# Kernel optimization log

Hardware: AMD Instinct MI355X
Metric: run time of the kernel (lower is better)

Reference implementation:

```python
import jax, jax.numpy as jnp
import numpy as np

N = 50000        # nodes
E = 800000       # edges (before self loops)
F_IN = 64        # num_features
DIM = 64         # num_hidden
C = 10           # num_classes
G = 256          # graphs in batch
NEG_SLOPE = 0.2


def setup_inputs() -> dict:
    key = jax.random.key(0)
    ks = jax.random.split(key, 20)
    def w(k, shape, fan_in):
        return jax.random.normal(k, shape, dtype=jnp.float32) / np.sqrt(fan_in)
    x = jax.random.normal(ks[0], (N, F_IN), dtype=jnp.float32)
    edge_index = jax.random.randint(ks[1], (2, E), 0, N, dtype=jnp.int64)
    batch = jnp.sort(jax.random.randint(ks[2], (N,), 0, G, dtype=jnp.int64))
    return {
        "x": x, "edge_index": edge_index, "batch": batch,
        "w1": w(ks[3], (F_IN, DIM), F_IN), "as1": w(ks[4], (DIM,), DIM), "ad1": w(ks[5], (DIM,), DIM), "b1": jnp.zeros((DIM,), jnp.float32),
        "w2": w(ks[6], (DIM, DIM), DIM),  "as2": w(ks[7], (DIM,), DIM), "ad2": w(ks[8], (DIM,), DIM), "b2": jnp.zeros((DIM,), jnp.float32),
        "w3": w(ks[9], (DIM, DIM), DIM),  "as3": w(ks[10], (DIM,), DIM), "ad3": w(ks[11], (DIM,), DIM), "b3": jnp.zeros((DIM,), jnp.float32),
        "fc1_w": w(ks[12], (DIM, DIM), DIM), "fc1_b": jnp.zeros((DIM,), jnp.float32),
        "fc2_w": w(ks[13], (DIM, C), DIM),   "fc2_b": jnp.zeros((C,), jnp.float32),
    }


def _gat_conv(x, src, dst, w, a_src, a_dst, b, n_nodes):
    # PyG GATConv, heads=1: h = x W; e_ij = LeakyReLU(a_src.h_j + a_dst.h_i);
    # alpha = segment-softmax over edges grouped by target i; out_i = sum_j alpha_ij h_j + b
    h = x @ w                                   # [N, DIM]
    alpha_s = h @ a_src                         # [N]
    alpha_d = h @ a_dst                         # [N]
    e = jax.nn.leaky_relu(alpha_s[src] + alpha_d[dst], NEG_SLOPE)  # [E']
    e_max = jax.ops.segment_max(e, dst, num_segments=n_nodes)
    e_exp = jnp.exp(e - e_max[dst])
    denom = jax.ops.segment_sum(e_exp, dst, num_segments=n_nodes)
    alpha = e_exp / (denom[dst] + 1e-16)        # [E']
    out = jax.ops.segment_sum(alpha[:, None] * h[src], dst, num_segments=n_nodes)
    return out + b


def _l2_normalize(x):
    nrm = jnp.linalg.norm(x, axis=1, keepdims=True)
    return x / jnp.maximum(nrm, 1e-12)


def reference(x, edge_index, batch, w1, as1, ad1, b1, w2, as2, ad2, b2,
              w3, as3, ad3, b3, fc1_w, fc1_b, fc2_w, fc2_b):
    n = x.shape[0]
    loops = jnp.arange(n, dtype=edge_index.dtype)
    src = jnp.concatenate([edge_index[0], loops])   # add_self_loops=True (PyG default)
    dst = jnp.concatenate([edge_index[1], loops])
    h = _gat_conv(x, src, dst, w1, as1, ad1, b1, n)
    h = jax.nn.relu(_l2_normalize(h))
    h = _gat_conv(h, src, dst, w2, as2, ad2, b2, n)
    h = jax.nn.relu(_l2_normalize(h))
    h = _gat_conv(h, src, dst, w3, as3, ad3, b3, n)
    h = jax.nn.relu(_l2_normalize(h))
    g = jax.ops.segment_sum(h, batch, num_segments=G)   # global_add_pool -> [G, DIM]
    g = jax.nn.relu(g @ fc1_w + fc1_b)
    logits = g @ fc2_w + fc2_b
    return jax.nn.log_softmax(logits, axis=-1)
```

## Files before the change

kernel.cpp:

```cpp
#include <hip/hip_runtime.h>
#include <hip/hip_bf16.h>
#include <math.h>

#define DIM 64
#define GNUM 256
#define CNUM 10

__device__ __forceinline__ unsigned bfpack(float a, float b) {
    unsigned ua = __builtin_bit_cast(unsigned, a);
    unsigned ub = __builtin_bit_cast(unsigned, b);
    ua += 0x7fffu + ((ua >> 16) & 1u);
    ub += 0x7fffu + ((ub >> 16) & 1u);
    return (ua >> 16) | (ub & 0xffff0000u);
}
__device__ __forceinline__ float bflo(unsigned u) { return __builtin_bit_cast(float, u << 16); }
__device__ __forceinline__ float bfhi(unsigned u) { return __builtin_bit_cast(float, u & 0xffff0000u); }
__device__ __forceinline__ float bfs(unsigned short u) { return __builtin_bit_cast(float, (unsigned)u << 16); }

__global__ void deg_rank_kernel(const int* __restrict__ ei, int E, int N,
                                int* __restrict__ deg, int* __restrict__ rank) {
    int i = blockIdx.x * blockDim.x + threadIdx.x;
    int EP = E + N;
    if (i >= EP) return;
    int d = (i < E) ? ei[E + i] : (i - E);
    rank[i] = atomicAdd(&deg[d], 1);
}

__global__ __launch_bounds__(256) void scan_misc(const int* __restrict__ deg, int* __restrict__ part, int n, int nb,
                                                 const int* __restrict__ batch, int N,
                                                 int* __restrict__ gstart) {
    int bid = blockIdx.x;
    if (bid < nb) {
        __shared__ int ws[4];
        int i = bid * 256 + threadIdx.x;
        int v = (i < n) ? deg[i] : 0;
        #pragma unroll
        for (int d = 32; d >= 1; d >>= 1) v += __shfl_xor(v, d);
        if ((threadIdx.x & 63) == 0) ws[threadIdx.x >> 6] = v;
        __syncthreads();
        if (threadIdx.x == 0) part[bid] = ws[0] + ws[1] + ws[2] + ws[3];
    } else {
        for (int g = threadIdx.x; g <= GNUM; g += 256) {
            int lo = 0, hi = N;
            while (lo < hi) { int mid = (lo + hi) >> 1; if (batch[mid] < g) lo = mid + 1; else hi = mid; }
            gstart[g] = lo;
        }
    }
}

__global__ __launch_bounds__(256) void scan_down(const int* __restrict__ deg, const int* __restrict__ part,
                                                 int* __restrict__ offs, int n) {
    __shared__ int ws[4];
    __shared__ int base_s;
    int tid = threadIdx.x, lane = tid & 63, wid = tid >> 6;
    int pv = (tid < (int)blockIdx.x) ? part[tid] : 0;
    #pragma unroll
    for (int d = 32; d >= 1; d >>= 1) pv += __shfl_xor(pv, d);
    if (lane == 0) ws[wid] = pv;
    __syncthreads();
    if (tid == 0) base_s = ws[0] + ws[1] + ws[2] + ws[3];
    __syncthreads();
    int i = blockIdx.x * 256 + tid;
    int v = (i < n) ? deg[i] : 0;
    int x = v;
    #pragma unroll
    for (int d = 1; d < 64; d <<= 1) { int t = __shfl_up(x, d); if (lane >= d) x += t; }
    if (lane == 63) ws[wid] = x;
    __syncthreads();
    int add = base_s;
    for (int w = 0; w < wid; ++w) add += ws[w];
    if (i < n) offs[i] = add + x - v;
    if (i == n - 1) offs[n] = add + x;
}

#define XSTR 68
__device__ __forceinline__ void mm_core_512(const float* __restrict__ xT, const float* __restrict__ Ws,
                                            const float* __restrict__ a_s, const float* __restrict__ a_d,
                                            unsigned* __restrict__ hbn, float* __restrict__ asn,
                                            float* __restrict__ adn, int base, int N) {
    int tid = threadIdx.x;
    int tx = tid & 15, ty = tid >> 4;
    int c0 = tx << 2, r0 = ty << 1;
    float acc[2][4] = {{0.f}};
    #pragma unroll 8
    for (int k = 0; k < DIM; ++k) {
        float2 xv = *(const float2*)(xT + k * XSTR + r0);
        float4 wv = *(const float4*)(Ws + k * DIM + c0);
        acc[0][0] += xv.x * wv.x; acc[0][1] += xv.x * wv.y; acc[0][2] += xv.x * wv.z; acc[0][3] += xv.x * wv.w;
        acc[1][0] += xv.y * wv.x; acc[1][1] += xv.y * wv.y; acc[1][2] += xv.y * wv.z; acc[1][3] += xv.y * wv.w;
    }
    float4 av = *(const float4*)(a_s + c0);
    float4 dv = *(const float4*)(a_d + c0);
    #pragma unroll
    for (int ri = 0; ri < 2; ++ri) {
        int grow = base + r0 + ri;
        float s1 = acc[ri][0] * av.x + acc[ri][1] * av.y + acc[ri][2] * av.z + acc[ri][3] * av.w;
        float s2 = acc[ri][0] * dv.x + acc[ri][1] * dv.y + acc[ri][2] * dv.z + acc[ri][3] * dv.w;
        #pragma unroll
        for (int d = 1; d <= 8; d <<= 1) { s1 += __shfl_xor(s1, d); s2 += __shfl_xor(s2, d); }
        if (grow < N) {
            uint2 o;
            o.x = bfpack(acc[ri][0], acc[ri][1]);
            o.y = bfpack(acc[ri][2], acc[ri][3]);
            *(uint2*)(hbn + ((size_t)grow << 5) + (tx << 1)) = o;
            if (tx == 0) { asn[grow] = s1; adn[grow] = s2; }
        }
    }
}

__global__ __launch_bounds__(512) void mm_fill(const float* __restrict__ in, const float* __restrict__ W,
                                               const float* __restrict__ a_s, const float* __restrict__ a_d,
                                               unsigned* __restrict__ hb, float* __restrict__ as_,
                                               float* __restrict__ ad_, int N, int nbt,
                                               const int* __restrict__ ei, const int* __restrict__ rank, int E,
                                               const int* __restrict__ offs, int2* __restrict__ csr_sd) {
    int bid = blockIdx.x;
    if (bid < nbt) {
        __shared__ float Ws[DIM * DIM];
        __shared__ float xT[XSTR * DIM];
        int tid = threadIdx.x;
        int base = bid * 64;

        const float4* W4 = (const float4*)W;
        float4* Ws4 = (float4*)Ws;
        Ws4[tid] = W4[tid];
        Ws4[tid + 512] = W4[tid + 512];

        {
            int row = tid >> 3;
            int kb = (tid & 7) << 3;
            int grow = base + row;
            int crow = grow < N ? grow : N - 1;
            const float4* xr = (const float4*)(in + ((size_t)crow << 6) + kb);
            float4 v0 = xr[0], v1 = xr[1];
            xT[(kb + 0) * XSTR + row] = v0.x;  xT[(kb + 1) * XSTR + row] = v0.y;
            xT[(kb + 2) * XSTR + row] = v0.z;  xT[(kb + 3) * XSTR + row] = v0.w;
            xT[(kb + 4) * XSTR + row] = v1.x;  xT[(kb + 5) * XSTR + row] = v1.y;
            xT[(kb + 6) * XSTR + row] = v1.z;  xT[(kb + 7) * XSTR + row] = v1.w;
        }
        __syncthreads();
        mm_core_512(xT, Ws, a_s, a_d, hb, as_, ad_, base, N);
    } else {
        int i = (bid - nbt) * 512 + threadIdx.x;
        int EP = E + N;
        if (i >= EP) return;
        int s, d;
        if (i < E) { s = ei[i]; d = ei[E + i]; } else { s = i - E; d = i - E; }
        csr_sd[offs[d] + rank[i]] = make_int2(s, d);
    }
}

#define FUS_NPB 64
#define FUS_CAP 2560
__global__ __launch_bounds__(512) void agg_mm(const unsigned* __restrict__ hbp,
                                              const int2* __restrict__ csr_sd,
                                              const float* __restrict__ asp,
                                              const float* __restrict__ adp,
                                              const int* __restrict__ offs,
                                              const float* __restrict__ bias,
                                              const float* __restrict__ W,
                                              const float* __restrict__ a_s,
                                              const float* __restrict__ a_d,
                                              unsigned* __restrict__ hbn,
                                              float* __restrict__ asn,
                                              float* __restrict__ adn, int N) {
    __shared__ int soffs[FUS_NPB + 1];
    __shared__ float adl[FUS_NPB];
    __shared__ int2 lsw[FUS_CAP + 4];
    __shared__ float xT[XSTR * DIM];
    float* Ws = (float*)lsw;

    int tid = threadIdx.x;
    int base = blockIdx.x * FUS_NPB;
    if (tid <= FUS_NPB) {
        int n = base + tid;
        soffs[tid] = offs[n < N ? n : N];
    }
    if (tid < FUS_NPB) {
        int n = base + tid;
        adl[tid] = (n < N) ? adp[n] : 0.f;
    }
    __syncthreads();
    int estart = soffs[0];
    int nE = soffs[FUS_NPB] - estart;
    bool inLds = (nE <= FUS_CAP);
    if (inLds) {
        for (int i = tid; i < nE; i += 512) {
            int2 sd = csr_sd[estart + i];
            float e = asp[sd.x] + adl[sd.y - base];
            e = (e > 0.f) ? e : 0.2f * e;
            lsw[i] = make_int2(sd.x, __builtin_bit_cast(int, expf(e)));
        }
        if (tid < 4) lsw[nE + tid] = make_int2(0, 0);
    }
    __syncthreads();

    int li = tid >> 3, fg = tid & 7;
    int node = base + li;
    int ls = soffs[li] - estart;
    int deg = soffs[li + 1] - soffs[li];

    float a0 = 0.f, a1 = 0.f, a2 = 0.f, a3 = 0.f;
    float a4 = 0.f, a5 = 0.f, a6 = 0.f, a7 = 0.f, sw = 0.f;
    if (inLds) {
        for (int eb = 0; eb < deg; eb += 4) {
            int t = ls + eb;
            int2 eA = lsw[t], eB = lsw[t + 1], eC = lsw[t + 2], eD = lsw[t + 3];
            float wA = __builtin_bit_cast(float, eA.y);
            float wB = (eb + 1 < deg) ? __builtin_bit_cast(float, eB.y) : 0.f;
            float wC = (eb + 2 < deg) ? __builtin_bit_cast(float, eC.y) : 0.f;
            float wD = (eb + 3 < deg) ? __builtin_bit_cast(float, eD.y) : 0.f;
            const uint4 hA = *(const uint4*)(hbp + ((size_t)eA.x << 5) + (fg << 2));
            const uint4 hB = *(const uint4*)(hbp + ((size_t)eB.x << 5) + (fg << 2));
            const uint4 hC = *(const uint4*)(hbp + ((size_t)eC.x << 5) + (fg << 2));
            const uint4 hD = *(const uint4*)(hbp + ((size_t)eD.x << 5) + (fg << 2));
            sw += wA + wB + wC + wD;
            a0 += wA * bflo(hA.x) + wB * bflo(hB.x) + wC * bflo(hC.x) + wD * bflo(hD.x);
            a1 += wA * bfhi(hA.x) + wB * bfhi(hB.x) + wC * bfhi(hC.x) + wD * bfhi(hD.x);
            a2 += wA * bflo(hA.y) + wB * bflo(hB.y) + wC * bflo(hC.y) + wD * bflo(hD.y);
            a3 += wA * bfhi(hA.y) + wB * bfhi(hB.y) + wC * bfhi(hC.y) + wD * bfhi(hD.y);
            a4 += wA * bflo(hA.z) + wB * bflo(hB.z) + wC * bflo(hC.z) + wD * bflo(hD.z);
            a5 += wA * bfhi(hA.z) + wB * bfhi(hB.z) + wC * bfhi(hC.z) + wD * bfhi(hD.z);
            a6 += wA * bflo(hA.w) + wB * bflo(hB.w) + wC * bflo(hC.w) + wD * bflo(hD.w);
            a7 += wA * bfhi(hA.w) + wB * bfhi(hB.w) + wC * bfhi(hC.w) + wD * bfhi(hD.w);
        }
    } else {
        float adi = adl[li];
        for (int eb = 0; eb < deg; eb += 4) {
            int t = estart + ls + eb;
            float wv[4]; int sv[4];
            #pragma unroll
            for (int k = 0; k < 4; ++k) {
                int2 sd = (eb + k < deg) ? csr_sd[t + k] : make_int2(0, 0);
                int s = sd.x; s = s < 0 ? 0 : (s >= N ? N - 1 : s);
                float e = asp[s] + adi;
                e = (e > 0.f) ? e : 0.2f * e;
                wv[k] = (eb + k < deg) ? expf(e) : 0.f;
                sv[k] = s;
            }
            #pragma unroll
            for (int k = 0; k < 4; ++k) {
                const uint4 hv = *(const uint4*)(hbp + ((size_t)sv[k] << 5) + (fg << 2));
                sw += wv[k];
                a0 += wv[k] * bflo(hv.x); a1 += wv[k] * bfhi(hv.x);
                a2 += wv[k] * bflo(hv.y); a3 += wv[k] * bfhi(hv.y);
                a4 += wv[k] * bflo(hv.z); a5 += wv[k] * bfhi(hv.z);
                a6 += wv[k] * bflo(hv.w); a7 += wv[k] * bfhi(hv.w);
            }
        }
    }

    float inv = 1.f / (sw + 1e-16f);
    const float4 b0 = *(const float4*)(bias + (fg << 3));
    const float4 b1 = *(const float4*)(bias + (fg << 3) + 4);
    float o0 = a0 * inv + b0.x, o1 = a1 * inv + b0.y, o2 = a2 * inv + b0.z, o3 = a3 * inv + b0.w;
    float o4 = a4 * inv + b1.x, o5 = a5 * inv + b1.y, o6 = a6 * inv + b1.z, o7 = a7 * inv + b1.w;
    float n2 = o0 * o0 + o1 * o1 + o2 * o2 + o3 * o3 + o4 * o4 + o5 * o5 + o6 * o6 + o7 * o7;
    #pragma unroll
    for (int d = 1; d <= 4; d <<= 1) n2 += __shfl_xor(n2, d);
    float innrm = 1.f / fmaxf(sqrtf(n2), 1e-12f);
    if (node >= N) innrm = 0.f;
    int kb = fg << 3;
    xT[(kb + 0) * XSTR + li] = fmaxf(o0 * innrm, 0.f);
    xT[(kb + 1) * XSTR + li] = fmaxf(o1 * innrm, 0.f);
    xT[(kb + 2) * XSTR + li] = fmaxf(o2 * innrm, 0.f);
    xT[(kb + 3) * XSTR + li] = fmaxf(o3 * innrm, 0.f);
    xT[(kb + 4) * XSTR + li] = fmaxf(o4 * innrm, 0.f);
    xT[(kb + 5) * XSTR + li] = fmaxf(o5 * innrm, 0.f);
    xT[(kb + 6) * XSTR + li] = fmaxf(o6 * innrm, 0.f);
    xT[(kb + 7) * XSTR + li] = fmaxf(o7 * innrm, 0.f);
    __syncthreads();

    const float4* W4 = (const float4*)W;
    float4* Ws4 = (float4*)Ws;
    Ws4[tid] = W4[tid];
    Ws4[tid + 512] = W4[tid + 512];
    __syncthreads();
    mm_core_512(xT, Ws, a_s, a_d, hbn, asn, adn, base, N);
}

#define AGG_NPB 64
#define AGG_CAP 2560
__global__ __launch_bounds__(512) void gat_agg(const unsigned* __restrict__ hb,
                                               const int2* __restrict__ csr_sd,
                                               const float* __restrict__ as_,
                                               const float* __restrict__ ad_,
                                               const int* __restrict__ offs,
                                               const float* __restrict__ bias,
                                               unsigned* __restrict__ outb, int N) {
    __shared__ int soffs[AGG_NPB + 1];
    __shared__ float adl[AGG_NPB];
    __shared__ int2 lsw[AGG_CAP + 4];
    int tid = threadIdx.x;
    int base = blockIdx.x * AGG_NPB;
    if (tid <= AGG_NPB) {
        int n = base + tid;
        soffs[tid] = offs[n < N ? n : N];
    }
    if (tid < AGG_NPB) {
        int n = base + tid;
        adl[tid] = (n < N) ? ad_[n] : 0.f;
    }
    __syncthreads();
    int estart = soffs[0];
    int nE = soffs[AGG_NPB] - estart;
    bool inLds = (nE <= AGG_CAP);
    if (inLds) {
        for (int i = tid; i < nE; i += 512) {
            int2 sd = csr_sd[estart + i];
            float e = as_[sd.x] + adl[sd.y - base];
            e = (e > 0.f) ? e : 0.2f * e;
            lsw[i] = make_int2(sd.x, __builtin_bit_cast(int, expf(e)));
        }
        if (tid < 4) lsw[nE + tid] = make_int2(0, 0);
    }
    __syncthreads();

    int li = tid >> 3, fg = tid & 7;
    int node = base + li;
    int ls = soffs[li] - estart;
    int deg = soffs[li + 1] - soffs[li];

    float a0 = 0.f, a1 = 0.f, a2 = 0.f, a3 = 0.f;
    float a4 = 0.f, a5 = 0.f, a6 = 0.f, a7 = 0.f, sw = 0.f;
    if (inLds) {
        for (int eb = 0; eb < deg; eb += 4) {
            int t = ls + eb;
            int2 eA = lsw[t], eB = lsw[t + 1], eC = lsw[t + 2], eD = lsw[t + 3];
            float wA = __builtin_bit_cast(float, eA.y);
            float wB = (eb + 1 < deg) ? __builtin_bit_cast(float, eB.y) : 0.f;
            float wC = (eb + 2 < deg) ? __builtin_bit_cast(float, eC.y) : 0.f;
            float wD = (eb + 3 < deg) ? __builtin_bit_cast(float, eD.y) : 0.f;
            const uint4 hA = *(const uint4*)(hb + ((size_t)eA.x << 5) + (fg << 2));
            const uint4 hB = *(const uint4*)(hb + ((size_t)eB.x << 5) + (fg << 2));
            const uint4 hC = *(const uint4*)(hb + ((size_t)eC.x << 5) + (fg << 2));
            const uint4 hD = *(const uint4*)(hb + ((size_t)eD.x << 5) + (fg << 2));
            sw += wA + wB + wC + wD;
            a0 += wA * bflo(hA.x) + wB * bflo(hB.x) + wC * bflo(hC.x) + wD * bflo(hD.x);
            a1 += wA * bfhi(hA.x) + wB * bfhi(hB.x) + wC * bfhi(hC.x) + wD * bfhi(hD.x);
            a2 += wA * bflo(hA.y) + wB * bflo(hB.y) + wC * bflo(hC.y) + wD * bflo(hD.y);
            a3 += wA * bfhi(hA.y) + wB * bfhi(hB.y) + wC * bfhi(hC.y) + wD * bfhi(hD.y);
            a4 += wA * bflo(hA.z) + wB * bflo(hB.z) + wC * bflo(hC.z) + wD * bflo(hD.z);
            a5 += wA * bfhi(hA.z) + wB * bfhi(hB.z) + wC * bfhi(hC.z) + wD * bfhi(hD.z);
            a6 += wA * bflo(hA.w) + wB * bflo(hB.w) + wC * bflo(hC.w) + wD * bflo(hD.w);
            a7 += wA * bfhi(hA.w) + wB * bfhi(hB.w) + wC * bfhi(hC.w) + wD * bfhi(hD.w);
        }
    } else {
        float adi = (node < N) ? ad_[node] : 0.f;
        for (int eb = 0; eb < deg; eb += 4) {
            int t = estart + ls + eb;
            float wv[4]; int sv[4];
            #pragma unroll
            for (int k = 0; k < 4; ++k) {
                int2 sd = (eb + k < deg) ? csr_sd[t + k] : make_int2(0, 0);
                int s = sd.x; s = s < 0 ? 0 : (s >= N ? N - 1 : s);
                float e = as_[s] + adi;
                e = (e > 0.f) ? e : 0.2f * e;
                wv[k] = (eb + k < deg) ? expf(e) : 0.f;
                sv[k] = s;
            }
            #pragma unroll
            for (int k = 0; k < 4; ++k) {
                const uint4 hv = *(const uint4*)(hb + ((size_t)sv[k] << 5) + (fg << 2));
                sw += wv[k];
                a0 += wv[k] * bflo(hv.x); a1 += wv[k] * bfhi(hv.x);
                a2 += wv[k] * bflo(hv.y); a3 += wv[k] * bfhi(hv.y);
                a4 += wv[k] * bflo(hv.z); a5 += wv[k] * bfhi(hv.z);
                a6 += wv[k] * bflo(hv.w); a7 += wv[k] * bfhi(hv.w);
            }
        }
    }

    float inv = 1.f / (sw + 1e-16f);
    const float4 b0 = *(const float4*)(bias + (fg << 3));
    const float4 b1 = *(const float4*)(bias + (fg << 3) + 4);
    float o0 = a0 * inv + b0.x, o1 = a1 * inv + b0.y, o2 = a2 * inv + b0.z, o3 = a3 * inv + b0.w;
    float o4 = a4 * inv + b1.x, o5 = a5 * inv + b1.y, o6 = a6 * inv + b1.z, o7 = a7 * inv + b1.w;
    float n2 = o0 * o0 + o1 * o1 + o2 * o2 + o3 * o3 + o4 * o4 + o5 * o5 + o6 * o6 + o7 * o7;
    #pragma unroll
    for (int d = 1; d <= 4; d <<= 1) n2 += __shfl_xor(n2, d);
    float innrm = 1.f / fmaxf(sqrtf(n2), 1e-12f);
    if (node < N) {
        uint4 o;
        o.x = bfpack(fmaxf(o0 * innrm, 0.f), fmaxf(o1 * innrm, 0.f));
        o.y = bfpack(fmaxf(o2 * innrm, 0.f), fmaxf(o3 * innrm, 0.f));
        o.z = bfpack(fmaxf(o4 * innrm, 0.f), fmaxf(o5 * innrm, 0.f));
        o.w = bfpack(fmaxf(o6 * innrm, 0.f), fmaxf(o7 * innrm, 0.f));
        *(uint4*)(outb + ((size_t)node << 5) + (fg << 2)) = o;
    }
}

__global__ __launch_bounds__(256) void pool_mlp(const unsigned short* __restrict__ hb, const int* __restrict__ gstart,
                                                const float* __restrict__ fc1w, const float* __restrict__ fc1b,
                                                const float* __restrict__ fc2w, const float* __restrict__ fc2b,
                                                float* __restrict__ out) {
    __shared__ float W1[DIM * DIM];
    __shared__ float red[4 * DIM];
    __shared__ float tbuf[DIM];
    __shared__ float obuf[CNUM];
    int tid = threadIdx.x, lane = tid & 63, wv = tid >> 6;
    int gid = blockIdx.x;

    const float4* W4 = (const float4*)fc1w;
    float4* W1s = (float4*)W1;
    #pragma unroll
    for (int i = 0; i < 4; ++i) W1s[tid + 256 * i] = W4[tid + 256 * i];

    int s = gstart[gid], e = gstart[gid + 1];
    float acc = 0.f;
    for (int i = s + wv; i < e; i += 4) acc += bfs(hb[((size_t)i << 6) + lane]);
    red[wv * DIM + lane] = acc;
    __syncthreads();

    if (wv == 0) {
        float g = red[lane] + red[DIM + lane] + red[2 * DIM + lane] + red[3 * DIM + lane];
        float t = fc1b[lane];
        #pragma unroll
        for (int k = 0; k < DIM; ++k) t += __shfl(g, k) * W1[k * DIM + lane];
        t = fmaxf(t, 0.f);
        tbuf[lane] = t;
        float o = 0.f;
        if (lane < CNUM) {
            o = fc2b[lane];
            #pragma unroll
            for (int k = 0; k < DIM; ++k) o += tbuf[k] * fc2w[k * CNUM + lane];
            obuf[lane] = o;
        }
        if (lane < CNUM) {
            float mx = obuf[0];
            #pragma unroll
            for (int k = 1; k < CNUM; ++k) mx = fmaxf(mx, obuf[k]);
            float ssum = 0.f;
            #pragma unroll
            for (int k = 0; k < CNUM; ++k) ssum += expf(obuf[k] - mx);
            out[gid * CNUM + lane] = o - mx - logf(ssum);
        }
    }
}

static inline size_t align256(size_t x) { return (x + 255) & ~size_t(255); }

extern "C" void kernel_launch(void* const* d_in, const int* in_sizes, int n_in,
                              void* d_out, int out_size, void* d_ws, size_t ws_size,
                              hipStream_t stream) {
    const float* x     = (const float*)d_in[0];
    const int*   ei    = (const int*)d_in[1];
    const int*   batch = (const int*)d_in[2];
    const float* w1  = (const float*)d_in[3];
    const float* as1 = (const float*)d_in[4];
    const float* ad1 = (const float*)d_in[5];
    const float* b1  = (const float*)d_in[6];
    const float* w2  = (const float*)d_in[7];
    const float* as2 = (const float*)d_in[8];
    const float* ad2 = (const float*)d_in[9];
    const float* b2  = (const float*)d_in[10];
    const float* w3  = (const float*)d_in[11];
    const float* as3 = (const float*)d_in[12];
    const float* ad3 = (const float*)d_in[13];
    const float* b3  = (const float*)d_in[14];
    const float* fc1w = (const float*)d_in[15];
    const float* fc1b = (const float*)d_in[16];
    const float* fc2w = (const float*)d_in[17];
    const float* fc2b = (const float*)d_in[18];
    float* out = (float*)d_out;

    int N  = in_sizes[0] / DIM;
    int E  = in_sizes[1] / 2;
    int EP = E + N;
    int nb = (N + 255) / 256;

    char* p = (char*)d_ws;
    unsigned* hbA = (unsigned*)p; p += align256(sizeof(unsigned) * (size_t)N * (DIM / 2));
    unsigned* hbB = (unsigned*)p; p += align256(sizeof(unsigned) * (size_t)N * (DIM / 2));
    unsigned* oAb = (unsigned*)p; p += align256(sizeof(unsigned) * (size_t)N * (DIM / 2));
    float* asA  = (float*)p; p += align256(sizeof(float) * (size_t)N);
    float* adA  = (float*)p; p += align256(sizeof(float) * (size_t)N);
    float* asB  = (float*)p; p += align256(sizeof(float) * (size_t)N);
    float* adB  = (float*)p; p += align256(sizeof(float) * (size_t)N);
    int*   deg  = (int*)p;   p += align256(sizeof(int) * (size_t)N);
    int*   offs = (int*)p;   p += align256(sizeof(int) * (size_t)(N + 1));
    int*   rank = (int*)p;   p += align256(sizeof(int) * (size_t)EP);
    int2*  csr_sd = (int2*)p; p += align256(sizeof(int2) * (size_t)EP);
    int*   part = (int*)p;   p += align256(sizeof(int) * (size_t)nb);
    int*   gst  = (int*)p;   p += align256(sizeof(int) * (size_t)(GNUM + 1));

    int nfb  = (N + FUS_NPB - 1) / FUS_NPB;
    int nblk = (N + AGG_NPB - 1) / AGG_NPB;
    int nbt = (N + 63) / 64;
    int epBlocks = (EP + 511) / 512;

    hipMemsetAsync(deg, 0, sizeof(int) * (size_t)N, stream);
    deg_rank_kernel<<<(EP + 255) / 256, 256, 0, stream>>>(ei, E, N, deg, rank);
    scan_misc<<<nb + 1, 256, 0, stream>>>(deg, part, N, nb, batch, N, gst);
    scan_down<<<nb, 256, 0, stream>>>(deg, part, offs, N);

    mm_fill<<<nbt + epBlocks, 512, 0, stream>>>(x, w1, as1, ad1, hbA, asA, adA, N, nbt,
                                                ei, rank, E, offs, csr_sd);
    agg_mm<<<nfb, 512, 0, stream>>>(hbA, csr_sd, asA, adA, offs, b1, w2, as2, ad2,
                                    hbB, asB, adB, N);
    agg_mm<<<nfb, 512, 0, stream>>>(hbB, csr_sd, asB, adB, offs, b2, w3, as3, ad3,
                                    hbA, asA, adA, N);
    gat_agg<<<nblk, 512, 0, stream>>>(hbA, csr_sd, asA, adA, offs, b3, oAb, N);

    pool_mlp<<<GNUM, 256, 0, stream>>>((const unsigned short*)oAb, gst, fc1w, fc1b, fc2w, fc2b, out);
}
```

Before: 253.5 us.

## Fuse last GAT aggregation with global pooling and MLP head via atomics

```diff
diff --git a/kernel.cpp b/kernel.cpp
--- a/kernel.cpp
+++ b/kernel.cpp
@@ -15,7 +15,6 @@
 }
 __device__ __forceinline__ float bflo(unsigned u) { return __builtin_bit_cast(float, u << 16); }
 __device__ __forceinline__ float bfhi(unsigned u) { return __builtin_bit_cast(float, u & 0xffff0000u); }
-__device__ __forceinline__ float bfs(unsigned short u) { return __builtin_bit_cast(float, (unsigned)u << 16); }
 
 __global__ void deg_rank_kernel(const int* __restrict__ ei, int E, int N,
                                 int* __restrict__ deg, int* __restrict__ rank) {
@@ -279,20 +278,63 @@
     mm_core_512(xT, Ws, a_s, a_d, hbn, asn, adn, base, N);
 }
 
+__device__ __forceinline__ void mlp_wave(int g, float gv, int lane,
+                                         const float* __restrict__ fc1w, const float* __restrict__ fc1b,
+                                         const float* __restrict__ fc2w, const float* __restrict__ fc2b,
+                                         float* __restrict__ out) {
+    float t = fc1b[lane];
+    #pragma unroll 8
+    for (int k = 0; k < DIM; ++k) t += __shfl(gv, k) * fc1w[k * DIM + lane];
+    t = fmaxf(t, 0.f);
+    float o = (lane < CNUM) ? fc2b[lane] : 0.f;
+    #pragma unroll 8
+    for (int k = 0; k < DIM; ++k) {
+        float tk = __shfl(t, k);
+        if (lane < CNUM) o += tk * fc2w[k * CNUM + lane];
+    }
+    float mx = -1e30f;
+    #pragma unroll
+    for (int c = 0; c < CNUM; ++c) mx = fmaxf(mx, __shfl(o, c));
+    float ss = 0.f;
+    #pragma unroll
+    for (int c = 0; c < CNUM; ++c) ss += expf(__shfl(o, c) - mx);
+    if (lane < CNUM) out[g * CNUM + lane] = o - mx - logf(ss);
+}
+
 #define AGG_NPB 64
 #define AGG_CAP 2560
-__global__ __launch_bounds__(512) void gat_agg(const unsigned* __restrict__ hb,
-                                               const int2* __restrict__ csr_sd,
-                                               const float* __restrict__ as_,
-                                               const float* __restrict__ ad_,
-                                               const int* __restrict__ offs,
-                                               const float* __restrict__ bias,
-                                               unsigned* __restrict__ outb, int N) {
+__global__ __launch_bounds__(512) void agg_pool(const unsigned* __restrict__ hb,
+                                                const int2* __restrict__ csr_sd,
+                                                const float* __restrict__ as_,
+                                                const float* __restrict__ ad_,
+                                                const int* __restrict__ offs,
+                                                const float* __restrict__ bias,
+                                                const int* __restrict__ batch,
+                                                const int* __restrict__ gstart,
+                                                float* __restrict__ gbuf,
+                                                int* __restrict__ gcnt,
+                                                const float* __restrict__ fc1w, const float* __restrict__ fc1b,
+                                                const float* __restrict__ fc2w, const float* __restrict__ fc2b,
+                                                float* __restrict__ out, int N, int nblk) {
+    if ((int)blockIdx.x == nblk) {
+        if (threadIdx.x < 64) {
+            int lane = threadIdx.x;
+            for (int g = 0; g < GNUM; ++g)
+                if (gstart[g + 1] == gstart[g])
+                    mlp_wave(g, 0.f, lane, fc1w, fc1b, fc2w, fc2b, out);
+        }
+        return;
+    }
     __shared__ int soffs[AGG_NPB + 1];
     __shared__ float adl[AGG_NPB];
     __shared__ int2 lsw[AGG_CAP + 4];
+    __shared__ float nodeout[64 * 66];
+    __shared__ int bgr[64];
+    __shared__ int fing[64];
+    __shared__ int nfin;
     int tid = threadIdx.x;
     int base = blockIdx.x * AGG_NPB;
+    if (tid == 0) nfin = 0;
     if (tid <= AGG_NPB) {
         int n = base + tid;
         soffs[tid] = offs[n < N ? n : N];
@@ -300,6 +342,7 @@
     if (tid < AGG_NPB) {
         int n = base + tid;
         adl[tid] = (n < N) ? ad_[n] : 0.f;
+        bgr[tid] = (n < N) ? batch[n] : -1;
     }
     __syncthreads();
     int estart = soffs[0];
@@ -346,7 +389,7 @@
             a7 += wA * bfhi(hA.w) + wB * bfhi(hB.w) + wC * bfhi(hC.w) + wD * bfhi(hD.w);
         }
     } else {
-        float adi = (node < N) ? ad_[node] : 0.f;
+        float adi = adl[li];
         for (int eb = 0; eb < deg; eb += 4) {
             int t = estart + ls + eb;
             float wv[4]; int sv[4];
@@ -380,60 +423,50 @@
     #pragma unroll
     for (int d = 1; d <= 4; d <<= 1) n2 += __shfl_xor(n2, d);
     float innrm = 1.f / fmaxf(sqrtf(n2), 1e-12f);
-    if (node < N) {
-        uint4 o;
-        o.x = bfpack(fmaxf(o0 * innrm, 0.f), fmaxf(o1 * innrm, 0.f));
-        o.y = bfpack(fmaxf(o2 * innrm, 0.f), fmaxf(o3 * innrm, 0.f));
-        o.z = bfpack(fmaxf(o4 * innrm, 0.f), fmaxf(o5 * innrm, 0.f));
-        o.w = bfpack(fmaxf(o6 * innrm, 0.f), fmaxf(o7 * innrm, 0.f));
-        *(uint4*)(outb + ((size_t)node << 5) + (fg << 2)) = o;
-    }
-}
-
-__global__ __launch_bounds__(256) void pool_mlp(const unsigned short* __restrict__ hb, const int* __restrict__ gstart,
-                                                const float* __restrict__ fc1w, const float* __restrict__ fc1b,
-                                                const float* __restrict__ fc2w, const float* __restrict__ fc2b,
-                                                float* __restrict__ out) {
-    __shared__ float W1[DIM * DIM];
-    __shared__ float red[4 * DIM];
-    __shared__ float tbuf[DIM];
-    __shared__ float obuf[CNUM];
-    int tid = threadIdx.x, lane = tid & 63, wv = tid >> 6;
-    int gid = blockIdx.x;
-
-    const float4* W4 = (const float4*)fc1w;
-    float4* W1s = (float4*)W1;
-    #pragma unroll
-    for (int i = 0; i < 4; ++i) W1s[tid + 256 * i] = W4[tid + 256 * i];
-
-    int s = gstart[gid], e = gstart[gid + 1];
-    float acc = 0.f;
-    for (int i = s + wv; i < e; i += 4) acc += bfs(hb[((size_t)i << 6) + lane]);
-    red[wv * DIM + lane] = acc;
-    __syncthreads();
-
-    if (wv == 0) {
-        float g = red[lane] + red[DIM + lane] + red[2 * DIM + lane] + red[3 * DIM + lane];
-        float t = fc1b[lane];
-        #pragma unroll
-        for (int k = 0; k < DIM; ++k) t += __shfl(g, k) * W1[k * DIM + lane];
-        t = fmaxf(t, 0.f);
-        tbuf[lane] = t;
-        float o = 0.f;
-        if (lane < CNUM) {
-            o = fc2b[lane];
-            #pragma unroll
-            for (int k = 0; k < DIM; ++k) o += tbuf[k] * fc2w[k * CNUM + lane];
-            obuf[lane] = o;
-        }
-        if (lane < CNUM) {
-            float mx = obuf[0];
-            #pragma unroll
-            for (int k = 1; k < CNUM; ++k) mx = fmaxf(mx, obuf[k]);
-            float ssum = 0.f;
-            #pragma unroll
-            for (int k = 0; k < CNUM; ++k) ssum += expf(obuf[k] - mx);
-            out[gid * CNUM + lane] = o - mx - logf(ssum);
+    if (node >= N) innrm = 0.f;
+    int co = fg << 3;
+    nodeout[li * 66 + co + 0] = fmaxf(o0 * innrm, 0.f);
+    nodeout[li * 66 + co + 1] = fmaxf(o1 * innrm, 0.f);
+    nodeout[li * 66 + co + 2] = fmaxf(o2 * innrm, 0.f);
+    nodeout[li * 66 + co + 3] = fmaxf(o3 * innrm, 0.f);
+    nodeout[li * 66 + co + 4] = fmaxf(o4 * innrm, 0.f);
+    nodeout[li * 66 + co + 5] = fmaxf(o5 * innrm, 0.f);
+    nodeout[li * 66 + co + 6] = fmaxf(o6 * innrm, 0.f);
+    nodeout[li * 66 + co + 7] = fmaxf(o7 * innrm, 0.f);
+    __syncthreads();
+
+    if (tid < 64) {
+        int lane = tid;
+        int nvalid = N - base; if (nvalid > 64) nvalid = 64;
+        int r = 0;
+        while (r < nvalid) {
+            int g = bgr[r];
+            int re = r;
+            while (re < nvalid && bgr[re] == g) ++re;
+            float s = 0.f;
+            for (int q = r; q < re; ++q) s += nodeout[q * 66 + lane];
+            atomicAdd(&gbuf[g * 64 + lane], s);
+            __threadfence();
+            if (lane == 0) {
+                int fb = gstart[g] >> 6;
+                int lb = (gstart[g + 1] - 1) >> 6;
+                int expected = lb - fb + 1;
+                int old = atomicAdd(&gcnt[g], 1);
+                if (old == expected - 1) { fing[nfin] = g; ++nfin; }
+            }
+            r = re;
+        }
+    }
+    __syncthreads();
+
+    if (tid < 64) {
+        int lane = tid;
+        int nf = nfin;
+        for (int fi = 0; fi < nf; ++fi) {
+            int g = fing[fi];
+            __threadfence();
+            float gv = __hip_atomic_load(&gbuf[g * 64 + lane], __ATOMIC_ACQUIRE, __HIP_MEMORY_SCOPE_AGENT);
+            mlp_wave(g, gv, lane, fc1w, fc1b, fc2w, fc2b, out);
         }
     }
 }
@@ -472,12 +505,15 @@
     char* p = (char*)d_ws;
     unsigned* hbA = (unsigned*)p; p += align256(sizeof(unsigned) * (size_t)N * (DIM / 2));
     unsigned* hbB = (unsigned*)p; p += align256(sizeof(unsigned) * (size_t)N * (DIM / 2));
-    unsigned* oAb = (unsigned*)p; p += align256(sizeof(unsigned) * (size_t)N * (DIM / 2));
     float* asA  = (float*)p; p += align256(sizeof(float) * (size_t)N);
     float* adA  = (float*)p; p += align256(sizeof(float) * (size_t)N);
     float* asB  = (float*)p; p += align256(sizeof(float) * (size_t)N);
     float* adB  = (float*)p; p += align256(sizeof(float) * (size_t)N);
-    int*   deg  = (int*)p;   p += align256(sizeof(int) * (size_t)N);
+    char* zstart = p;
+    int*      deg  = (int*)p;      p += align256(sizeof(int) * (size_t)N);
+    int*      gcnt = (int*)p;      p += align256(sizeof(int) * (size_t)GNUM);
+    float*    gbuf = (float*)p;    p += align256(sizeof(float) * (size_t)GNUM * DIM);
+    char* zend = p;
     int*   offs = (int*)p;   p += align256(sizeof(int) * (size_t)(N + 1));
     int*   rank = (int*)p;   p += align256(sizeof(int) * (size_t)EP);
     int2*  csr_sd = (int2*)p; p += align256(sizeof(int2) * (size_t)EP);
@@ -489,7 +525,7 @@
     int nbt = (N + 63) / 64;
     int epBlocks = (EP + 511) / 512;
 
-    hipMemsetAsync(deg, 0, sizeof(int) * (size_t)N, stream);
+    hipMemsetAsync(zstart, 0, (size_t)(zend - zstart), stream);
     deg_rank_kernel<<<(EP + 255) / 256, 256, 0, stream>>>(ei, E, N, deg, rank);
     scan_misc<<<nb + 1, 256, 0, stream>>>(deg, part, N, nb, batch, N, gst);
     scan_down<<<nb, 256, 0, stream>>>(deg, part, offs, N);
@@ -500,7 +536,6 @@
                                     hbB, asB, adB, N);
     agg_mm<<<nfb, 512, 0, stream>>>(hbB, csr_sd, asB, adB, offs, b2, w3, as3, ad3,
                                     hbA, asA, adA, N);
-    gat_agg<<<nblk, 512, 0, stream>>>(hbA, csr_sd, asA, adA, offs, b3, oAb, N);
-
-    pool_mlp<<<GNUM, 256, 0, stream>>>((const unsigned short*)oAb, gst, fc1w, fc1b, fc2w, fc2b, out);
-}
+    agg_pool<<<nblk + 1, 512, 0, stream>>>(hbA, csr_sd, asA, adA, offs, b3, batch, gst,
+                                           gbuf, gcnt, fc1w, fc1b, fc2w, fc2b, out, N, nblk);
+}
```

Result: slower. 268.8 us (+6.0%).
